# Kernel optimization log

Hardware: AMD Instinct MI355X
Metric: run time of the kernel (lower is better)

## Reference

```python
import jax, jax.numpy as jnp
import numpy as np

IN_DIM = 256
BOTTLENECK = 32
QK_DIM = IN_DIM // BOTTLENECK  # 8


def setup_inputs() -> dict:
    key = jax.random.key(0)
    ks = jax.random.split(key, 10)
    B, C, W, H = 4, IN_DIM, 64, 64
    s = 0.05
    return {
        "x": jax.random.normal(ks[0], (B, C, W, H), jnp.float32),
        "k": jax.random.normal(ks[1], (B, C, W, H), jnp.float32),
        "q": jax.random.normal(ks[2], (B, C, W, H), jnp.float32),
        "Wq": jax.random.normal(ks[3], (QK_DIM, C), jnp.float32) * s,
        "bq": jax.random.normal(ks[4], (QK_DIM,), jnp.float32) * s,
        "Wk": jax.random.normal(ks[5], (QK_DIM, C), jnp.float32) * s,
        "bk": jax.random.normal(ks[6], (QK_DIM,), jnp.float32) * s,
        "Wv": jax.random.normal(ks[7], (C, C), jnp.float32) * s,
        "bv": jax.random.normal(ks[8], (C,), jnp.float32) * s,
        "gamma": jnp.array([0.5], jnp.float32),
    }


def reference(x, k, q, Wq, bq, Wk, bk, Wv, bv, gamma):
    B, C, W, H = x.shape
    N = W * H
    # 1x1 convs == per-pixel linear maps over channels; flatten spatial to N
    xf = x.reshape(B, C, N)
    kf = k.reshape(B, C, N)
    qf = q.reshape(B, C, N)
    # proj_query: (B, N, d); proj_key: (B, d, N)
    pq = jnp.einsum('dc,bcn->bnd', Wq, qf) + bq[None, None, :]
    pk = jnp.einsum('dc,bcn->bdn', Wk, kf) + bk[None, :, None]
    energy = jnp.einsum('bnd,bdm->bnm', pq, pk)  # (B, N, N), un-scaled
    attention = jax.nn.softmax(energy, axis=-1)
    pv = jnp.einsum('ec,bcn->ben', Wv, xf) + bv[None, :, None]  # (B, C, N)
    # out = bmm(value, attention^T): out[b,c,n] = sum_m pv[b,c,m] * attn[b,n,m]
    out = jnp.einsum('bcm,bnm->bcn', pv, attention)
    out = out.reshape(B, C, W, H)
    out = gamma[0] * out + x
    return out, attention
```

## Files before the change

### kernel.cpp

```cpp
#include <hip/hip_runtime.h>

#define B_ 4
#define C_ 256
#define N_ 4096
#define D_ 8

typedef float f32x4 __attribute__((ext_vector_type(4)));
typedef __bf16 bf16x8 __attribute__((ext_vector_type(8)));

union U16 {
  bf16x8 v;
  unsigned short u[8];
  uint4 q;
};

__device__ inline unsigned short f2bf(float f) {
  unsigned int u = __float_as_uint(f);
  u = (u + 0x7FFFu + ((u >> 16) & 1u)) >> 16;
  return (unsigned short)u;
}

__global__ void __launch_bounds__(256) k_pqk(
    const float* __restrict__ q, const float* __restrict__ k,
    const float* __restrict__ Wq, const float* __restrict__ bq,
    const float* __restrict__ Wk, const float* __restrict__ bk,
    float* __restrict__ pq_g, float* __restrict__ pk_g) {
  int b = blockIdx.y, n0 = blockIdx.x * 64;
  int t = threadIdx.x, nl = t & 63, sub = t >> 6;
  int n = n0 + nl;
  float aq[D_], ak[D_];
#pragma unroll
  for (int d = 0; d < D_; ++d) { aq[d] = 0.f; ak[d] = 0.f; }
  const float* qp = q + ((size_t)(b * C_ + sub * 64)) * N_ + n;
  const float* kp = k + ((size_t)(b * C_ + sub * 64)) * N_ + n;
  for (int cc = 0; cc < 64; ++cc) {
    int c = sub * 64 + cc;
    float qv = qp[(size_t)cc * N_];
    float kv = kp[(size_t)cc * N_];
#pragma unroll
    for (int d = 0; d < D_; ++d) {
      aq[d] = fmaf(Wq[d * C_ + c], qv, aq[d]);
      ak[d] = fmaf(Wk[d * C_ + c], kv, ak[d]);
    }
  }
  __shared__ float red[4][64][16];
#pragma unroll
  for (int d = 0; d < D_; ++d) { red[sub][nl][d] = aq[d]; red[sub][nl][8 + d] = ak[d]; }
  __syncthreads();
  if (t < 64) {
#pragma unroll
    for (int d = 0; d < D_; ++d) {
      float s = red[0][t][d] + red[1][t][d] + red[2][t][d] + red[3][t][d] + bq[d];
      pq_g[((size_t)b * N_ + n0 + t) * D_ + d] = s;
      float s2 = red[0][t][8 + d] + red[1][t][8 + d] + red[2][t][8 + d] + red[3][t][8 + d] + bk[d];
      pk_g[((size_t)b * D_ + d) * N_ + n0 + t] = s2;
    }
  }
}

__global__ void __launch_bounds__(256) k_pv(
    const float* __restrict__ x, const float* __restrict__ Wv,
    const float* __restrict__ bv, unsigned short* __restrict__ pvF) {
  int b = blockIdx.y, n0 = blockIdx.x * 64;
  int t = threadIdx.x, lane = t & 63, w = t >> 6;
  __shared__ unsigned short xs[64][264];
  {
    int nl = t & 63, sub = t >> 6;
    for (int i = 0; i < 64; ++i) {
      int c = i * 4 + sub;
      float xv = x[((size_t)(b * C_ + c)) * N_ + n0 + nl];
      xs[nl][c] = f2bf(xv);
    }
  }
  __syncthreads();
  int e0 = w * 64;
  f32x4 acc[4][4];
#pragma unroll
  for (int mf = 0; mf < 4; ++mf)
#pragma unroll
    for (int nf = 0; nf < 4; ++nf) acc[mf][nf] = (f32x4)0.f;

  int rsel = lane & 15, koff = (lane >> 4) * 8;
  for (int kc = 0; kc < 8; ++kc) {
    int cbase = kc * 32 + koff;
    U16 afr[4];
#pragma unroll
    for (int mf = 0; mf < 4; ++mf) {
      const float* wp = Wv + (size_t)(e0 + mf * 16 + rsel) * C_ + cbase;
      float4 w0 = *(const float4*)wp;
      float4 w1 = *(const float4*)(wp + 4);
      afr[mf].u[0] = f2bf(w0.x); afr[mf].u[1] = f2bf(w0.y);
      afr[mf].u[2] = f2bf(w0.z); afr[mf].u[3] = f2bf(w0.w);
      afr[mf].u[4] = f2bf(w1.x); afr[mf].u[5] = f2bf(w1.y);
      afr[mf].u[6] = f2bf(w1.z); afr[mf].u[7] = f2bf(w1.w);
    }
    U16 bfr[4];
#pragma unroll
    for (int nf = 0; nf < 4; ++nf)
      bfr[nf].q = *(const uint4*)&xs[nf * 16 + rsel][cbase];
#pragma unroll
    for (int mf = 0; mf < 4; ++mf)
#pragma unroll
      for (int nf = 0; nf < 4; ++nf)
        acc[mf][nf] = __builtin_amdgcn_mfma_f32_16x16x32_bf16(afr[mf].v, bfr[nf].v, acc[mf][nf], 0, 0, 0);
  }
  unsigned short* pvFb = pvF + (size_t)b * C_ * N_;
  int rowsub = (lane >> 4) * 4;
#pragma unroll
  for (int mf = 0; mf < 4; ++mf) {
#pragma unroll
    for (int nf = 0; nf < 4; ++nf) {
      int n = n0 + nf * 16 + rsel;
      int tt = n >> 6, m_in = n & 63;
      int kf = m_in >> 5, rr2 = m_in & 31, g2 = rr2 >> 3, j2 = rr2 & 7;
#pragma unroll
      for (int j = 0; j < 4; ++j) {
        int e = e0 + mf * 16 + rowsub + j;
        float v = acc[mf][nf][j] + bv[e];
        int cg = e >> 4, cl = e & 15;
        size_t word = ((size_t)(tt * 16 + cg) * 2 + kf) * 64 + g2 * 16 + cl;
        pvFb[word * 8 + j2] = f2bf(v);
      }
    }
  }
}

__global__ void __launch_bounds__(256) k_rowsum(
    const float* __restrict__ pq_g, const float* __restrict__ pk_g,
    float* __restrict__ rinv_g) {
  int b = blockIdx.y, n0 = blockIdx.x * 32;
  int t = threadIdx.x, lane = t & 63, w = t >> 6;
  int r0 = n0 + w * 8;
  float pqr[8][D_];
#pragma unroll
  for (int r = 0; r < 8; ++r) {
    const float4* pp = (const float4*)(pq_g + ((size_t)b * N_ + r0 + r) * D_);
    float4 a = pp[0], c4 = pp[1];
    pqr[r][0] = a.x; pqr[r][1] = a.y; pqr[r][2] = a.z; pqr[r][3] = a.w;
    pqr[r][4] = c4.x; pqr[r][5] = c4.y; pqr[r][6] = c4.z; pqr[r][7] = c4.w;
  }
  float s[8];
#pragma unroll
  for (int r = 0; r < 8; ++r) s[r] = 0.f;
  const float* pkb = pk_g + (size_t)b * D_ * N_;
  for (int tt = 0; tt < 64; ++tt) {
    int m = tt * 64 + lane;
    float pkr[D_];
#pragma unroll
    for (int d = 0; d < D_; ++d) pkr[d] = pkb[(size_t)d * N_ + m];
#pragma unroll
    for (int r = 0; r < 8; ++r) {
      float e = pqr[r][0] * pkr[0];
#pragma unroll
      for (int d = 1; d < D_; ++d) e = fmaf(pqr[r][d], pkr[d], e);
      s[r] += __expf(e);
    }
  }
#pragma unroll
  for (int r = 0; r < 8; ++r) {
    float v = s[r];
    for (int off = 32; off; off >>= 1) v += __shfl_xor(v, off);
    s[r] = v;
  }
  if (lane == 0) {
#pragma unroll
    for (int r = 0; r < 8; ++r) rinv_g[(size_t)b * N_ + r0 + r] = 1.0f / s[r];
  }
}

__global__ void __launch_bounds__(256, 4) k_fused(
    const float* __restrict__ pq_g, const float* __restrict__ pk_g,
    const float* __restrict__ rinv_g, const unsigned short* __restrict__ pvF,
    const float* __restrict__ x, const float* __restrict__ gamma,
    float* __restrict__ out_g, float* __restrict__ attn_g) {
  int bx = blockIdx.x;
  int b = bx & 3, grp = bx >> 2;
  int n0 = grp * 16;
  int t = threadIdx.x, lane = t & 63, w = t >> 6;
  int rsel = lane & 15, g = lane >> 4, koff = g * 8;
  int c0 = w * 64;
  int r0 = n0 + w * 4;

  __shared__ unsigned short asl[2][16][72];

  float pqr[4][D_], rinv[4];
#pragma unroll
  for (int rr = 0; rr < 4; ++rr) {
    const float4* pp = (const float4*)(pq_g + ((size_t)b * N_ + r0 + rr) * D_);
    float4 a = pp[0], c4 = pp[1];
    pqr[rr][0] = a.x; pqr[rr][1] = a.y; pqr[rr][2] = a.z; pqr[rr][3] = a.w;
    pqr[rr][4] = c4.x; pqr[rr][5] = c4.y; pqr[rr][6] = c4.z; pqr[rr][7] = c4.w;
    rinv[rr] = rinv_g[(size_t)b * N_ + r0 + rr];
  }

  const float* pkb = pk_g + (size_t)b * D_ * N_;
  const unsigned short* pvFb = pvF + (size_t)b * C_ * N_;
  float* attb = attn_g + ((size_t)b * N_ + r0) * N_;

  f32x4 acc[4];
#pragma unroll
  for (int cf = 0; cf < 4; ++cf) acc[cf] = (f32x4)0.f;

  float pkr[D_];
#pragma unroll
  for (int d = 0; d < D_; ++d) pkr[d] = pkb[(size_t)d * N_ + lane];

  int cur = 0;
  for (int tt = 0; tt < 64; ++tt) {
    int m0 = tt * 64;
    bool more = (tt + 1 < 64);
    float pkn[D_];
    if (more) {
#pragma unroll
      for (int d = 0; d < D_; ++d) pkn[d] = pkb[(size_t)d * N_ + m0 + 64 + lane];
    }
#pragma unroll
    for (int rr = 0; rr < 4; ++rr) {
      float e = pqr[rr][0] * pkr[0];
#pragma unroll
      for (int d = 1; d < D_; ++d) e = fmaf(pqr[rr][d], pkr[d], e);
      float a = __expf(e) * rinv[rr];
      __builtin_nontemporal_store(a, attb + (size_t)rr * N_ + m0 + lane);
      asl[cur][w * 4 + rr][lane] = f2bf(a);
    }
    asm volatile("s_waitcnt lgkmcnt(0)" ::: "memory");
    __builtin_amdgcn_s_barrier();
    {
      U16 afr[2], bfr[2][4];
#pragma unroll
      for (int kf = 0; kf < 2; ++kf) {
        afr[kf].q = *(const uint4*)&asl[cur][rsel][kf * 32 + koff];
#pragma unroll
        for (int cf = 0; cf < 4; ++cf) {
          int cg = (c0 >> 4) + cf;
          bfr[kf][cf].q = *(const uint4*)(pvFb +
              (((size_t)(tt * 16 + cg) * 2 + kf) * 64 + lane) * 8);
        }
      }
#pragma unroll
      for (int kf = 0; kf < 2; ++kf)
#pragma unroll
        for (int cf = 0; cf < 4; ++cf)
          acc[cf] = __builtin_amdgcn_mfma_f32_16x16x32_bf16(
              afr[kf].v, bfr[kf][cf].v, acc[cf], 0, 0, 0);
    }
#pragma unroll
    for (int d = 0; d < D_; ++d) pkr[d] = pkn[d];
    cur ^= 1;
  }
  float gm = gamma[0];
  int rowsub = g * 4;
#pragma unroll
  for (int cf = 0; cf < 4; ++cf) {
    int c = c0 + cf * 16 + rsel;
    int nrow = n0 + rowsub;
    const float4 xv = *(const float4*)(x + ((size_t)(b * C_ + c)) * N_ + nrow);
    float4 o;
    o.x = gm * acc[cf][0] + xv.x;
    o.y = gm * acc[cf][1] + xv.y;
    o.z = gm * acc[cf][2] + xv.z;
    o.w = gm * acc[cf][3] + xv.w;
    *(float4*)(out_g + ((size_t)(b * C_ + c)) * N_ + nrow) = o;
  }
}

extern "C" void kernel_launch(void* const* d_in, const int* in_sizes, int n_in,
                              void* d_out, int out_size, void* d_ws, size_t ws_size,
                              hipStream_t stream) {
  const float* x  = (const float*)d_in[0];
  const float* k  = (const float*)d_in[1];
  const float* q  = (const float*)d_in[2];
  const float* Wq = (const float*)d_in[3];
  const float* bq = (const float*)d_in[4];
  const float* Wk = (const float*)d_in[5];
  const float* bk = (const float*)d_in[6];
  const float* Wv = (const float*)d_in[7];
  const float* bv = (const float*)d_in[8];
  const float* gamma = (const float*)d_in[9];

  float* out_g  = (float*)d_out;
  float* attn_g = out_g + (size_t)B_ * C_ * N_;

  char* ws = (char*)d_ws;
  float* pq_g = (float*)ws;
  float* pk_g = (float*)(ws + (1u << 19));
  float* rinv_g = (float*)(ws + (1u << 20));
  unsigned short* pvF = (unsigned short*)(ws + (1u << 20) + (1u << 17));

  k_pqk<<<dim3(64, B_), 256, 0, stream>>>(q, k, Wq, bq, Wk, bk, pq_g, pk_g);
  k_pv<<<dim3(64, B_), 256, 0, stream>>>(x, Wv, bv, pvF);
  k_rowsum<<<dim3(128, B_), 256, 0, stream>>>(pq_g, pk_g, rinv_g);
  k_fused<<<dim3(1024), 256, 0, stream>>>(pq_g, pk_g, rinv_g, pvF, x, gamma, out_g, attn_g);
}
```

Baseline: 199.7 us.

## Retile fused attention kernel to 32 rows by 128 channels per block

Each block now covers 32 query rows and half of the channels (128), with each wave owning 8 rows and 32 channels as a 2x2 set of MFMA tiles, instead of 16 rows and all 256 channels. The pv fragment loads move to the start of each iteration so they overlap the exp computation. Because each pv fragment is now reused across two row tiles, pv traffic per row drops. The cost is that the exp/energy work is duplicated across the two channel halves, with only the ch==0 block writing the attention output. Occupancy is lowered to 3 blocks per CU to make room for the extra registers.

Measured after the change: 196.5 us. About the same (-1.6%).

```diff
diff --git a/kernel.cpp b/kernel.cpp
--- a/kernel.cpp
+++ b/kernel.cpp
@@ -168,24 +168,26 @@
   }
 }
 
-__global__ void __launch_bounds__(256, 4) k_fused(
+__global__ void __launch_bounds__(256, 3) k_fused(
     const float* __restrict__ pq_g, const float* __restrict__ pk_g,
     const float* __restrict__ rinv_g, const unsigned short* __restrict__ pvF,
     const float* __restrict__ x, const float* __restrict__ gamma,
     float* __restrict__ out_g, float* __restrict__ attn_g) {
   int bx = blockIdx.x;
-  int b = bx & 3, grp = bx >> 2;
-  int n0 = grp * 16;
+  int b = bx & 3;
+  int rest = bx >> 2;
+  int ch = rest & 1, grp = rest >> 1;
+  int n0 = grp * 32;
   int t = threadIdx.x, lane = t & 63, w = t >> 6;
   int rsel = lane & 15, g = lane >> 4, koff = g * 8;
-  int c0 = w * 64;
-  int r0 = n0 + w * 4;
-
-  __shared__ unsigned short asl[2][16][72];
-
-  float pqr[4][D_], rinv[4];
-#pragma unroll
-  for (int rr = 0; rr < 4; ++rr) {
+  int c0 = ch * 128 + w * 32;
+  int r0 = n0 + w * 8;
+
+  __shared__ unsigned short asl[2][32][72];
+
+  float pqr[8][D_], rinv[8];
+#pragma unroll
+  for (int rr = 0; rr < 8; ++rr) {
     const float4* pp = (const float4*)(pq_g + ((size_t)b * N_ + r0 + rr) * D_);
     float4 a = pp[0], c4 = pp[1];
     pqr[rr][0] = a.x; pqr[rr][1] = a.y; pqr[rr][2] = a.z; pqr[rr][3] = a.w;
@@ -197,9 +199,11 @@
   const unsigned short* pvFb = pvF + (size_t)b * C_ * N_;
   float* attb = attn_g + ((size_t)b * N_ + r0) * N_;
 
-  f32x4 acc[4];
-#pragma unroll
-  for (int cf = 0; cf < 4; ++cf) acc[cf] = (f32x4)0.f;
+  f32x4 acc[2][2];
+#pragma unroll
+  for (int mf = 0; mf < 2; ++mf)
+#pragma unroll
+    for (int cf = 0; cf < 2; ++cf) acc[mf][cf] = (f32x4)0.f;
 
   float pkr[D_];
 #pragma unroll
@@ -209,40 +213,47 @@
   for (int tt = 0; tt < 64; ++tt) {
     int m0 = tt * 64;
     bool more = (tt + 1 < 64);
+    U16 bfr[2][2];
+#pragma unroll
+    for (int kf = 0; kf < 2; ++kf)
+#pragma unroll
+      for (int cf = 0; cf < 2; ++cf) {
+        int cg = (c0 >> 4) + cf;
+        bfr[kf][cf].q = *(const uint4*)(pvFb +
+            (((size_t)(tt * 16 + cg) * 2 + kf) * 64 + lane) * 8);
+      }
     float pkn[D_];
     if (more) {
 #pragma unroll
       for (int d = 0; d < D_; ++d) pkn[d] = pkb[(size_t)d * N_ + m0 + 64 + lane];
     }
 #pragma unroll
-    for (int rr = 0; rr < 4; ++rr) {
+    for (int rr = 0; rr < 8; ++rr) {
       float e = pqr[rr][0] * pkr[0];
 #pragma unroll
       for (int d = 1; d < D_; ++d) e = fmaf(pqr[rr][d], pkr[d], e);
       float a = __expf(e) * rinv[rr];
-      __builtin_nontemporal_store(a, attb + (size_t)rr * N_ + m0 + lane);
-      asl[cur][w * 4 + rr][lane] = f2bf(a);
+      if (ch == 0)
+        __builtin_nontemporal_store(a, attb + (size_t)rr * N_ + m0 + lane);
+      asl[cur][w * 8 + rr][lane] = f2bf(a);
     }
     asm volatile("s_waitcnt lgkmcnt(0)" ::: "memory");
     __builtin_amdgcn_s_barrier();
     {
-      U16 afr[2], bfr[2][4];
-#pragma unroll
-      for (int kf = 0; kf < 2; ++kf) {
-        afr[kf].q = *(const uint4*)&asl[cur][rsel][kf * 32 + koff];
-#pragma unroll
-        for (int cf = 0; cf < 4; ++cf) {
-          int cg = (c0 >> 4) + cf;
-          bfr[kf][cf].q = *(const uint4*)(pvFb +
-              (((size_t)(tt * 16 + cg) * 2 + kf) * 64 + lane) * 8);
-        }
-      }
+      U16 afr[2][2];
 #pragma unroll
       for (int kf = 0; kf < 2; ++kf)
 #pragma unroll
-        for (int cf = 0; cf < 4; ++cf)
-          acc[cf] = __builtin_amdgcn_mfma_f32_16x16x32_bf16(
-              afr[kf].v, bfr[kf][cf].v, acc[cf], 0, 0, 0);
+        for (int mf = 0; mf < 2; ++mf)
+          afr[kf][mf].q = *(const uint4*)&asl[cur][mf * 16 + rsel][kf * 32 + koff];
+#pragma unroll
+      for (int kf = 0; kf < 2; ++kf)
+#pragma unroll
+        for (int mf = 0; mf < 2; ++mf)
+#pragma unroll
+          for (int cf = 0; cf < 2; ++cf)
+            acc[mf][cf] = __builtin_amdgcn_mfma_f32_16x16x32_bf16(
+                afr[kf][mf].v, bfr[kf][cf].v, acc[mf][cf], 0, 0, 0);
     }
 #pragma unroll
     for (int d = 0; d < D_; ++d) pkr[d] = pkn[d];
@@ -251,16 +262,19 @@
   float gm = gamma[0];
   int rowsub = g * 4;
 #pragma unroll
-  for (int cf = 0; cf < 4; ++cf) {
-    int c = c0 + cf * 16 + rsel;
-    int nrow = n0 + rowsub;
-    const float4 xv = *(const float4*)(x + ((size_t)(b * C_ + c)) * N_ + nrow);
-    float4 o;
-    o.x = gm * acc[cf][0] + xv.x;
-    o.y = gm * acc[cf][1] + xv.y;
-    o.z = gm * acc[cf][2] + xv.z;
-    o.w = gm * acc[cf][3] + xv.w;
-    *(float4*)(out_g + ((size_t)(b * C_ + c)) * N_ + nrow) = o;
+  for (int mf = 0; mf < 2; ++mf) {
+#pragma unroll
+    for (int cf = 0; cf < 2; ++cf) {
+      int c = c0 + cf * 16 + rsel;
+      int nrow = n0 + mf * 16 + rowsub;
+      const float4 xv = *(const float4*)(x + ((size_t)(b * C_ + c)) * N_ + nrow);
+      float4 o;
+      o.x = gm * acc[mf][cf][0] + xv.x;
+      o.y = gm * acc[mf][cf][1] + xv.y;
+      o.z = gm * acc[mf][cf][2] + xv.z;
+      o.w = gm * acc[mf][cf][3] + xv.w;
+      *(float4*)(out_g + ((size_t)(b * C_ + c)) * N_ + nrow) = o;
+    }
   }
 }
 
```
